# Kernel optimization log

Measured on AMD Instinct MI355X. Metric: run time of the kernel, lower is better.

The kernel has to match this reference:

```python
import jax, jax.numpy as jnp
import numpy as np

EMBED = 2048
N_EXPERTS = 64
TOP_K = 8


def setup_inputs() -> dict:
    key = jax.random.key(0)
    k_x, k_w, k_b = jax.random.split(key, 3)
    inputs = jax.random.normal(k_x, (8, 4096, EMBED), dtype=jnp.float32)
    # nn.Linear(embed_size, num_experts): weight [E, D], bias [E]
    bound = 1.0 / np.sqrt(EMBED)
    W = jax.random.uniform(k_w, (N_EXPERTS, EMBED), dtype=jnp.float32, minval=-bound, maxval=bound)
    b = jax.random.uniform(k_b, (N_EXPERTS,), dtype=jnp.float32, minval=-bound, maxval=bound)
    return {"inputs": inputs, "W": W, "b": b}


def reference(inputs, W, b):
    # scores: [B, S, E]
    scores = jnp.einsum("bsd,ed->bse", inputs, W) + b
    topk_scores, indices = jax.lax.top_k(scores, TOP_K)  # [B,S,K]
    # scatter topk_scores into a zero mask (non-selected slots stay 0.0)
    onehot = jax.nn.one_hot(indices, N_EXPERTS, dtype=scores.dtype)  # [B,S,K,E]
    mask = jnp.einsum("bske,bsk->bse", onehot, topk_scores)
    router_output = jax.nn.softmax(mask, axis=-1)
    return (router_output, indices)
```

## Files before the change

kernel.cpp:

```cpp
#include <hip/hip_runtime.h>
#include <math.h>

#define N_TOKENS 32768
#define EMBED    2048
#define NEXP     64
#define TOPK     8
#define BM       64
#define BK       64
#define D4       (EMBED / 4)
#define SCS      65
#define THRESH   1e-4f

typedef __attribute__((ext_vector_type(8)))  short short8;
typedef __attribute__((ext_vector_type(16))) float f32x16;

__device__ inline unsigned short bf16rne(float f) {
  unsigned int fb = __float_as_uint(f);
  return (unsigned short)((fb + 0x7FFFu + ((fb >> 16) & 1u)) >> 16);
}

__device__ inline void cvt8(float4 a, float4 b, short8& h, short8& l) {
  float fs[8] = {a.x, a.y, a.z, a.w, b.x, b.y, b.z, b.w};
#pragma unroll
  for (int i = 0; i < 8; ++i) {
    unsigned int hr = (__float_as_uint(fs[i]) + 0x7FFFu + ((__float_as_uint(fs[i]) >> 16) & 1u)) >> 16;
    h[i] = (short)hr;
    float hf = __uint_as_float(hr << 16);
    l[i] = (short)bf16rne(fs[i] - hf);
  }
}

__global__ __launch_bounds__(256, 2)
void router_kernel(const float* __restrict__ x, const float* __restrict__ W,
                   const float* __restrict__ bias, float* __restrict__ out) {
  __shared__ short xs_h[8 * 64 * 8], xs_l[8 * 64 * 8];
  __shared__ short ws_h[8 * 64 * 8], ws_l[8 * 64 * 8];
  __shared__ float sc[BM * SCS];
  __shared__ double s_fix[NEXP];
  __shared__ int s_list[BM];
  __shared__ int s_cnt;

  const int tid  = threadIdx.x;
  const int t0   = blockIdx.x * BM;
  const int lane = tid & 63;
  const int w    = tid >> 6;
  const int half = lane >> 5;
  const int r5   = lane & 31;
  const int tw   = (w & 1) * 32;
  const int ew   = (w >> 1) * 32;

  if (tid == 0) s_cnt = 0;

  const float4* x4 = (const float4*)x;
  const float4* W4 = (const float4*)W;
  const int stok = tid & 63;
  const float4* xrow = x4 + (size_t)(t0 + stok) * D4 + w * 4;
  const float4* wrow = W4 + (size_t)stok * D4 + w * 4;

  f32x16 acc;
#pragma unroll
  for (int i = 0; i < 16; ++i) acc[i] = 0.f;

  float4 px[4], pw[4];
#pragma unroll
  for (int i = 0; i < 4; ++i) { px[i] = xrow[i]; pw[i] = wrow[i]; }

  const int nch = EMBED / BK;
  for (int ch = 0; ch < nch; ++ch) {
    __syncthreads();
    {
      short8 h0, l0, h1, l1;
      cvt8(px[0], px[1], h0, l0); cvt8(px[2], px[3], h1, l1);
      *(short8*)&xs_h[((2 * w    ) * 64 + stok) * 8] = h0;
      *(short8*)&xs_h[((2 * w + 1) * 64 + stok) * 8] = h1;
      *(short8*)&xs_l[((2 * w    ) * 64 + stok) * 8] = l0;
      *(short8*)&xs_l[((2 * w + 1) * 64 + stok) * 8] = l1;
      cvt8(pw[0], pw[1], h0, l0); cvt8(pw[2], pw[3], h1, l1);
      *(short8*)&ws_h[((2 * w    ) * 64 + stok) * 8] = h0;
      *(short8*)&ws_h[((2 * w + 1) * 64 + stok) * 8] = h1;
      *(short8*)&ws_l[((2 * w    ) * 64 + stok) * 8] = l0;
      *(short8*)&ws_l[((2 * w + 1) * 64 + stok) * 8] = l1;
    }
    __syncthreads();

    if (ch + 1 < nch) {
      const int off = (ch + 1) * (BK / 4);
#pragma unroll
      for (int i = 0; i < 4; ++i) { px[i] = xrow[off + i]; pw[i] = wrow[off + i]; }
    }

#pragma unroll
    for (int s = 0; s < 4; ++s) {
      const int kg = s * 2 + half;
      short8 ah = *(const short8*)&xs_h[(kg * 64 + tw + r5) * 8];
      short8 al = *(const short8*)&xs_l[(kg * 64 + tw + r5) * 8];
      short8 bh = *(const short8*)&ws_h[(kg * 64 + ew + r5) * 8];
      short8 bl = *(const short8*)&ws_l[(kg * 64 + ew + r5) * 8];
      acc = __builtin_amdgcn_mfma_f32_32x32x16_bf16(ah, bh, acc, 0, 0, 0);
      acc = __builtin_amdgcn_mfma_f32_32x32x16_bf16(ah, bl, acc, 0, 0, 0);
      acc = __builtin_amdgcn_mfma_f32_32x32x16_bf16(al, bh, acc, 0, 0, 0);
    }
  }

#pragma unroll
  for (int reg = 0; reg < 16; ++reg) {
    const int row = (reg & 3) + 8 * (reg >> 2) + 4 * half;
    sc[(tw + row) * SCS + ew + r5] = acc[reg];
  }
  __syncthreads();

  float* rout = out;
  float* iout = out + (size_t)N_TOKENS * NEXP;
  const float bias_l = bias[lane];

  for (int tt = 0; tt < 16; ++tt) {
    const int t = w * 16 + tt;
    const float orig = sc[t * SCS + lane] + bias_l;
    unsigned int b = __float_as_uint(orig);
    unsigned int u = b ^ (((unsigned int)((int)b >> 31)) | 0x80000000u);
    const unsigned int key = (u & 0xFFFFFFC0u) | (63u - (unsigned int)lane);
    unsigned int cur = key;
    float fv[9];
    int myidx = 0; bool sel = false; float morig = 0.f;

#pragma unroll
    for (int r = 0; r < 9; ++r) {
      unsigned int v = cur;
#pragma unroll
      for (int s2 = 1; s2 < 64; s2 <<= 1) {
        unsigned int o = (unsigned int)__shfl_xor((int)v, s2);
        v = v > o ? v : o;
      }
      unsigned int vb = (v & 0x80000000u) ? (v ^ 0x80000000u) : ~v;
      fv[r] = __uint_as_float(vb);
      if (r < 8) {
        if (lane == r) myidx = 63 - (int)(v & 63u);
        if (cur == v) { sel = true; morig = orig; cur = 0u; }
      }
    }

    float ming = fv[0] - fv[1];
#pragma unroll
    for (int r = 1; r < 8; ++r) ming = fminf(ming, fv[r] - fv[r + 1]);

    if (ming < THRESH) {
      if (lane == 0) { int p = atomicAdd(&s_cnt, 1); s_list[p] = t; }
    } else {
      const float m = fmaxf(fv[0], 0.f);
      float Z = 56.f * expf(-m);
#pragma unroll
      for (int r = 0; r < 8; ++r) Z += expf(fv[r] - m);
      const float p = expf((sel ? morig : 0.f) - m) / Z;
      rout[(size_t)(t0 + t) * NEXP + lane] = p;
      if (lane < TOPK) iout[(size_t)(t0 + t) * TOPK + lane] = (float)myidx;
    }
  }

  __syncthreads();
  const int cnt = s_cnt;

  for (int i = 0; i < cnt; ++i) {
    const int t = s_list[i];
    const int e = tid >> 2, sub = tid & 3;
    const float4* xr = x4 + (size_t)(t0 + t) * D4 + sub * 128;
    const float4* wr = W4 + (size_t)e * D4 + sub * 128;
    double a0 = 0.0, a1 = 0.0;
#pragma unroll 4
    for (int m4 = 0; m4 < 128; m4 += 2) {
      float4 xv = xr[m4], wv = wr[m4];
      a0 = fma((double)xv.x, (double)wv.x, a0); a0 = fma((double)xv.y, (double)wv.y, a0);
      a0 = fma((double)xv.z, (double)wv.z, a0); a0 = fma((double)xv.w, (double)wv.w, a0);
      float4 xv2 = xr[m4 + 1], wv2 = wr[m4 + 1];
      a1 = fma((double)xv2.x, (double)wv2.x, a1); a1 = fma((double)xv2.y, (double)wv2.y, a1);
      a1 = fma((double)xv2.z, (double)wv2.z, a1); a1 = fma((double)xv2.w, (double)wv2.w, a1);
    }
    double a = a0 + a1;
    a += __shfl_xor(a, 1); a += __shfl_xor(a, 2);
    if (sub == 0) s_fix[e] = a + (double)bias[e];
    __syncthreads();

    if (tid < 64) {
      const double orig = s_fix[lane];
      double cur = orig, vals[8];
      int myidx = 0; double mym = 0.0;
#pragma unroll
      for (int r = 0; r < 8; ++r) {
        double v = cur; int id = lane;
#pragma unroll
        for (int s2 = 1; s2 < 64; s2 <<= 1) {
          const double ov = __shfl_xor(v, s2);
          const int    oi = __shfl_xor(id, s2);
          if (ov > v || (ov == v && oi < id)) { v = ov; id = oi; }
        }
        vals[r] = v;
        if (lane == r)  myidx = id;
        if (lane == id) { mym = orig; cur = -1e300; }
      }
      const double m = fmax(vals[0], 0.0);
      double Z = 56.0 * exp(-m);
#pragma unroll
      for (int r = 0; r < 8; ++r) Z += exp(vals[r] - m);
      const double p = exp(mym - m) / Z;
      rout[(size_t)(t0 + t) * NEXP + lane] = (float)p;
      if (lane < TOPK) iout[(size_t)(t0 + t) * TOPK + lane] = (float)myidx;
    }
    __syncthreads();
  }
}

extern "C" void kernel_launch(void* const* d_in, const int* in_sizes, int n_in,
                              void* d_out, int out_size, void* d_ws, size_t ws_size,
                              hipStream_t stream) {
  const float* x = (const float*)d_in[0];
  const float* W = (const float*)d_in[1];
  const float* b = (const float*)d_in[2];
  router_kernel<<<N_TOKENS / BM, 256, 0, stream>>>(x, W, b, (float*)d_out);
}
```

Measured before the change: 568.1 us.

## Pre-split W into bf16 hi/lo once and double-buffer swizzled X tiles

Adds a small pre-pass kernel that converts W into bf16 hi/lo halves in an MFMA-friendly layout in workspace. The main kernel then loads B fragments straight from global memory instead of converting W in every block. X tiles are double-buffered in LDS with an XOR swizzle, which removes one barrier per chunk and aims to cut bank conflicts. The top-k epilogue also processes four tokens at once to overlap shuffle latency. The cost is an extra kernel launch and more register pressure.

Result: no change. 558.8 us (-1.6%).

```diff
diff --git a/kernel.cpp b/kernel.cpp
--- a/kernel.cpp
+++ b/kernel.cpp
@@ -7,38 +7,57 @@
 #define TOPK     8
 #define BM       64
 #define BK       64
-#define D4       (EMBED / 4)
+#define NCH      (EMBED / BK)
 #define SCS      65
 #define THRESH   1e-4f
+#define WELEMS   (NEXP * EMBED)
 
 typedef __attribute__((ext_vector_type(8)))  short short8;
+typedef __attribute__((ext_vector_type(4)))  short short4v;
 typedef __attribute__((ext_vector_type(16))) float f32x16;
 
-__device__ inline unsigned short bf16rne(float f) {
+__device__ __forceinline__ unsigned short bf16rne(float f) {
   unsigned int fb = __float_as_uint(f);
   return (unsigned short)((fb + 0x7FFFu + ((fb >> 16) & 1u)) >> 16);
 }
 
-__device__ inline void cvt8(float4 a, float4 b, short8& h, short8& l) {
-  float fs[8] = {a.x, a.y, a.z, a.w, b.x, b.y, b.z, b.w};
-#pragma unroll
-  for (int i = 0; i < 8; ++i) {
-    unsigned int hr = (__float_as_uint(fs[i]) + 0x7FFFu + ((__float_as_uint(fs[i]) >> 16) & 1u)) >> 16;
-    h[i] = (short)hr;
-    float hf = __uint_as_float(hr << 16);
-    l[i] = (short)bf16rne(fs[i] - hf);
-  }
+__device__ __forceinline__ void cvt4(float4 f, short4v* h, short4v* l) {
+  float fs[4] = {f.x, f.y, f.z, f.w};
+  short4v hh, ll;
+#pragma unroll
+  for (int i = 0; i < 4; ++i) {
+    unsigned short hr = bf16rne(fs[i]);
+    hh[i] = (short)hr;
+    float hf = __uint_as_float((unsigned int)hr << 16);
+    ll[i] = (short)bf16rne(fs[i] - hf);
+  }
+  *h = hh; *l = ll;
+}
+
+__global__ void split_w(const float* __restrict__ W, short* __restrict__ wh,
+                        short* __restrict__ wl) {
+  const int T = blockIdx.x * 256 + threadIdx.x;
+  const int n = T >> 8, kg8 = T & 255;
+  const float4* W4 = (const float4*)W;
+  float4 a = W4[n * 512 + kg8 * 2];
+  float4 b = W4[n * 512 + kg8 * 2 + 1];
+  short4v h0, l0, h1, l1;
+  cvt4(a, &h0, &l0); cvt4(b, &h1, &l1);
+  short* dh = &wh[(kg8 * 64 + n) * 8];
+  short* dl = &wl[(kg8 * 64 + n) * 8];
+  *(short4v*)dh = h0; *(short4v*)(dh + 4) = h1;
+  *(short4v*)dl = l0; *(short4v*)(dl + 4) = l1;
 }
 
 __global__ __launch_bounds__(256, 2)
-void router_kernel(const float* __restrict__ x, const float* __restrict__ W,
-                   const float* __restrict__ bias, float* __restrict__ out) {
-  __shared__ short xs_h[8 * 64 * 8], xs_l[8 * 64 * 8];
-  __shared__ short ws_h[8 * 64 * 8], ws_l[8 * 64 * 8];
-  __shared__ float sc[BM * SCS];
+void router_kernel(const float* __restrict__ x, const short* __restrict__ wh,
+                   const short* __restrict__ wl, const float* __restrict__ bias,
+                   const float* __restrict__ Wf, float* __restrict__ out) {
+  __shared__ short  xs[2][2][8][64][8];
+  __shared__ float  sc[BM * SCS];
   __shared__ double s_fix[NEXP];
-  __shared__ int s_list[BM];
-  __shared__ int s_cnt;
+  __shared__ int    s_list[BM];
+  __shared__ int    s_cnt;
 
   const int tid  = threadIdx.x;
   const int t0   = blockIdx.x * BM;
@@ -51,54 +70,58 @@
 
   if (tid == 0) s_cnt = 0;
 
-  const float4* x4 = (const float4*)x;
-  const float4* W4 = (const float4*)W;
-  const int stok = tid & 63;
-  const float4* xrow = x4 + (size_t)(t0 + stok) * D4 + w * 4;
-  const float4* wrow = W4 + (size_t)stok * D4 + w * 4;
+  const int c4  = tid & 15;
+  const int rr  = tid >> 4;
+  const int g   = c4 >> 1;
+  const int sub = c4 & 1;
+
+  const float* xp = x + (size_t)(t0 + rr) * EMBED + (c4 << 2);
+  const short8* Bh = (const short8*)wh;
+  const short8* Bl = (const short8*)wl;
+  const int boff = half * 64 + ew + r5;
 
   f32x16 acc;
 #pragma unroll
   for (int i = 0; i < 16; ++i) acc[i] = 0.f;
 
-  float4 px[4], pw[4];
-#pragma unroll
-  for (int i = 0; i < 4; ++i) { px[i] = xrow[i]; pw[i] = wrow[i]; }
-
-  const int nch = EMBED / BK;
-  for (int ch = 0; ch < nch; ++ch) {
+  float4 px[4];
+#pragma unroll
+  for (int i = 0; i < 4; ++i)
+    px[i] = *(const float4*)(xp + (size_t)(i * 16) * EMBED);
+
+  for (int ch = 0; ch < NCH; ++ch) {
+    short8 bh[4], bl[4];
+#pragma unroll
+    for (int s = 0; s < 4; ++s) {
+      const int bi = (ch * 4 + s) * 128 + boff;
+      bh[s] = Bh[bi]; bl[s] = Bl[bi];
+    }
+    const int buf = ch & 1;
+#pragma unroll
+    for (int i = 0; i < 4; ++i) {
+      short4v h, l;
+      cvt4(px[i], &h, &l);
+      const int slot = (rr + 16 * i) ^ g;
+      *(short4v*)&xs[buf][0][g][slot][sub * 4] = h;
+      *(short4v*)&xs[buf][1][g][slot][sub * 4] = l;
+    }
     __syncthreads();
-    {
-      short8 h0, l0, h1, l1;
-      cvt8(px[0], px[1], h0, l0); cvt8(px[2], px[3], h1, l1);
-      *(short8*)&xs_h[((2 * w    ) * 64 + stok) * 8] = h0;
-      *(short8*)&xs_h[((2 * w + 1) * 64 + stok) * 8] = h1;
-      *(short8*)&xs_l[((2 * w    ) * 64 + stok) * 8] = l0;
-      *(short8*)&xs_l[((2 * w + 1) * 64 + stok) * 8] = l1;
-      cvt8(pw[0], pw[1], h0, l0); cvt8(pw[2], pw[3], h1, l1);
-      *(short8*)&ws_h[((2 * w    ) * 64 + stok) * 8] = h0;
-      *(short8*)&ws_h[((2 * w + 1) * 64 + stok) * 8] = h1;
-      *(short8*)&ws_l[((2 * w    ) * 64 + stok) * 8] = l0;
-      *(short8*)&ws_l[((2 * w + 1) * 64 + stok) * 8] = l1;
-    }
-    __syncthreads();
-
-    if (ch + 1 < nch) {
-      const int off = (ch + 1) * (BK / 4);
-#pragma unroll
-      for (int i = 0; i < 4; ++i) { px[i] = xrow[off + i]; pw[i] = wrow[off + i]; }
+
+    if (ch + 1 < NCH) {
+#pragma unroll
+      for (int i = 0; i < 4; ++i)
+        px[i] = *(const float4*)(xp + (size_t)(i * 16) * EMBED + (ch + 1) * BK);
     }
 
 #pragma unroll
     for (int s = 0; s < 4; ++s) {
-      const int kg = s * 2 + half;
-      short8 ah = *(const short8*)&xs_h[(kg * 64 + tw + r5) * 8];
-      short8 al = *(const short8*)&xs_l[(kg * 64 + tw + r5) * 8];
-      short8 bh = *(const short8*)&ws_h[(kg * 64 + ew + r5) * 8];
-      short8 bl = *(const short8*)&ws_l[(kg * 64 + ew + r5) * 8];
-      acc = __builtin_amdgcn_mfma_f32_32x32x16_bf16(ah, bh, acc, 0, 0, 0);
-      acc = __builtin_amdgcn_mfma_f32_32x32x16_bf16(ah, bl, acc, 0, 0, 0);
-      acc = __builtin_amdgcn_mfma_f32_32x32x16_bf16(al, bh, acc, 0, 0, 0);
+      const int kg   = 2 * s + half;
+      const int slot = (tw + r5) ^ kg;
+      short8 ah = *(const short8*)&xs[buf][0][kg][slot][0];
+      short8 al = *(const short8*)&xs[buf][1][kg][slot][0];
+      acc = __builtin_amdgcn_mfma_f32_32x32x16_bf16(ah, bh[s], acc, 0, 0, 0);
+      acc = __builtin_amdgcn_mfma_f32_32x32x16_bf16(ah, bl[s], acc, 0, 0, 0);
+      acc = __builtin_amdgcn_mfma_f32_32x32x16_bf16(al, bh[s], acc, 0, 0, 0);
     }
   }
 
@@ -113,57 +136,73 @@
   float* iout = out + (size_t)N_TOKENS * NEXP;
   const float bias_l = bias[lane];
 
-  for (int tt = 0; tt < 16; ++tt) {
-    const int t = w * 16 + tt;
-    const float orig = sc[t * SCS + lane] + bias_l;
-    unsigned int b = __float_as_uint(orig);
-    unsigned int u = b ^ (((unsigned int)((int)b >> 31)) | 0x80000000u);
-    const unsigned int key = (u & 0xFFFFFFC0u) | (63u - (unsigned int)lane);
-    unsigned int cur = key;
-    float fv[9];
-    int myidx = 0; bool sel = false; float morig = 0.f;
+  for (int tb = 0; tb < 4; ++tb) {
+    const int tbase = w * 16 + tb * 4;
+    float orig[4]; unsigned cur[4];
+#pragma unroll
+    for (int i = 0; i < 4; ++i) {
+      orig[i] = sc[(tbase + i) * SCS + lane] + bias_l;
+      unsigned b = __float_as_uint(orig[i]);
+      unsigned u = b ^ (((unsigned)((int)b >> 31)) | 0x80000000u);
+      cur[i] = (u & 0xFFFFFFC0u) | (63u - (unsigned)lane);
+    }
+    float m[4], Z[4], ming[4], prev[4], morig[4];
+    int myidx[4]; bool sel[4];
+#pragma unroll
+    for (int i = 0; i < 4; ++i) { sel[i] = false; morig[i] = 0.f; myidx[i] = 0; ming[i] = 1e30f; }
 
 #pragma unroll
     for (int r = 0; r < 9; ++r) {
-      unsigned int v = cur;
+      unsigned v[4];
+#pragma unroll
+      for (int i = 0; i < 4; ++i) v[i] = cur[i];
 #pragma unroll
       for (int s2 = 1; s2 < 64; s2 <<= 1) {
-        unsigned int o = (unsigned int)__shfl_xor((int)v, s2);
-        v = v > o ? v : o;
-      }
-      unsigned int vb = (v & 0x80000000u) ? (v ^ 0x80000000u) : ~v;
-      fv[r] = __uint_as_float(vb);
-      if (r < 8) {
-        if (lane == r) myidx = 63 - (int)(v & 63u);
-        if (cur == v) { sel = true; morig = orig; cur = 0u; }
-      }
-    }
-
-    float ming = fv[0] - fv[1];
-#pragma unroll
-    for (int r = 1; r < 8; ++r) ming = fminf(ming, fv[r] - fv[r + 1]);
-
-    if (ming < THRESH) {
-      if (lane == 0) { int p = atomicAdd(&s_cnt, 1); s_list[p] = t; }
-    } else {
-      const float m = fmaxf(fv[0], 0.f);
-      float Z = 56.f * expf(-m);
-#pragma unroll
-      for (int r = 0; r < 8; ++r) Z += expf(fv[r] - m);
-      const float p = expf((sel ? morig : 0.f) - m) / Z;
-      rout[(size_t)(t0 + t) * NEXP + lane] = p;
-      if (lane < TOPK) iout[(size_t)(t0 + t) * TOPK + lane] = (float)myidx;
+#pragma unroll
+        for (int i = 0; i < 4; ++i) {
+          unsigned o = (unsigned)__shfl_xor((int)v[i], s2);
+          v[i] = v[i] > o ? v[i] : o;
+        }
+      }
+#pragma unroll
+      for (int i = 0; i < 4; ++i) {
+        unsigned vb = (v[i] & 0x80000000u) ? (v[i] ^ 0x80000000u) : ~v[i];
+        float fv = __uint_as_float(vb);
+        if (r == 0) { m[i] = fmaxf(fv, 0.f); Z[i] = 56.f * expf(-m[i]) + expf(fv - m[i]); }
+        else {
+          ming[i] = fminf(ming[i], prev[i] - fv);
+          if (r < 8) Z[i] += expf(fv - m[i]);
+        }
+        prev[i] = fv;
+        if (r < 8) {
+          if (lane == r) myidx[i] = 63 - (int)(v[i] & 63u);
+          if (cur[i] == v[i]) { sel[i] = true; morig[i] = orig[i]; cur[i] = 0u; }
+        }
+      }
+    }
+#pragma unroll
+    for (int i = 0; i < 4; ++i) {
+      const int t = tbase + i;
+      if (ming[i] < THRESH) {
+        if (lane == 0) { int p = atomicAdd(&s_cnt, 1); s_list[p] = t; }
+      } else {
+        const float p = expf(morig[i] - m[i]) / Z[i];
+        rout[(size_t)(t0 + t) * NEXP + lane] = p;
+        if (lane < TOPK) iout[(size_t)(t0 + t) * TOPK + lane] = (float)myidx[i];
+      }
     }
   }
 
   __syncthreads();
   const int cnt = s_cnt;
+  const float4* x4 = (const float4*)x;
+  const float4* W4 = (const float4*)Wf;
 
   for (int i = 0; i < cnt; ++i) {
     const int t = s_list[i];
-    const int e = tid >> 2, sub = tid & 3;
-    const float4* xr = x4 + (size_t)(t0 + t) * D4 + sub * 128;
-    const float4* wr = W4 + (size_t)e * D4 + sub * 128;
+    const int e = tid >> 2, sub2 = tid & 3;
+    const float4* xr = x4 + (size_t)(t0 + t) * (EMBED / 4) + sub2 * 128;
+    const float4* wr = W4 + (size_t)e * (EMBED / 4) + sub2 * 128;
     double a0 = 0.0, a1 = 0.0;
 #pragma unroll 4
     for (int m4 = 0; m4 < 128; m4 += 2) {
@@ -176,16 +215,16 @@
     }
     double a = a0 + a1;
     a += __shfl_xor(a, 1); a += __shfl_xor(a, 2);
-    if (sub == 0) s_fix[e] = a + (double)bias[e];
+    if (sub2 == 0) s_fix[e] = a + (double)bias[e];
     __syncthreads();
 
     if (tid < 64) {
       const double orig = s_fix[lane];
-      double cur = orig, vals[8];
+      double curd = orig, vals[8];
       int myidx = 0; double mym = 0.0;
 #pragma unroll
       for (int r = 0; r < 8; ++r) {
-        double v = cur; int id = lane;
+        double v = curd; int id = lane;
 #pragma unroll
         for (int s2 = 1; s2 < 64; s2 <<= 1) {
           const double ov = __shfl_xor(v, s2);
@@ -194,13 +233,13 @@
         }
         vals[r] = v;
         if (lane == r)  myidx = id;
-        if (lane == id) { mym = orig; cur = -1e300; }
-      }
-      const double m = fmax(vals[0], 0.0);
-      double Z = 56.0 * exp(-m);
-#pragma unroll
-      for (int r = 0; r < 8; ++r) Z += exp(vals[r] - m);
-      const double p = exp(mym - m) / Z;
+        if (lane == id) { mym = orig; curd = -1e300; }
+      }
+      const double md = fmax(vals[0], 0.0);
+      double Zd = 56.0 * exp(-md);
+#pragma unroll
+      for (int r = 0; r < 8; ++r) Zd += exp(vals[r] - md);
+      const double p = exp(mym - md) / Zd;
       rout[(size_t)(t0 + t) * NEXP + lane] = (float)p;
       if (lane < TOPK) iout[(size_t)(t0 + t) * TOPK + lane] = (float)myidx;
     }
@@ -214,5 +253,8 @@
   const float* x = (const float*)d_in[0];
   const float* W = (const float*)d_in[1];
   const float* b = (const float*)d_in[2];
-  router_kernel<<<N_TOKENS / BM, 256, 0, stream>>>(x, W, b, (float*)d_out);
-}
+  short* wh = (short*)d_ws;
+  short* wl = wh + WELEMS;
+  split_w<<<64, 256, 0, stream>>>(W, wh, wl);
+  router_kernel<<<N_TOKENS / BM, 256, 0, stream>>>(x, wh, wl, b, W, (float*)d_out);
+}
```
